# Optimization experiments

Hardware: AMD Instinct MI355X
Metric: run time of the kernel (lower is better)

Reference implementation:

```python
import jax, jax.numpy as jnp
import numpy as np

B = 32; L = 512; D_MODEL = 512; N_LAYERS = 4
D_STATE = 64; D_CONV = 4; EXPAND = 2; HEADDIM = 64; PRED = 96
D_INNER = EXPAND * D_MODEL            # 1024
NHEADS = D_INNER // HEADDIM           # 16
CONV_DIM = D_INNER + 2 * D_STATE      # 1152
D_IN_PROJ = 2 * D_INNER + 2 * D_STATE + NHEADS  # 2192
EPS = 1e-5


def setup_inputs() -> dict:
    key = jax.random.key(0)
    ks = jax.random.split(key, 8)
    s = lambda k, shape, scale=0.02: jax.random.normal(k, shape, jnp.float32) * scale
    return {
        "x": jax.random.normal(ks[0], (B, L, D_MODEL), jnp.float32),
        "in_proj_w": s(ks[1], (N_LAYERS, D_IN_PROJ, D_MODEL)),
        "conv_w": s(ks[2], (N_LAYERS, CONV_DIM, D_CONV), 0.2),
        "conv_b": jnp.zeros((N_LAYERS, CONV_DIM), jnp.float32),
        "dt_bias": jnp.log(jnp.expm1(jax.random.uniform(ks[3], (N_LAYERS, NHEADS), minval=0.001, maxval=0.1))),
        "A_log": jnp.log(jax.random.uniform(ks[4], (N_LAYERS, NHEADS), minval=1.0, maxval=16.0)),
        "Dp": jnp.ones((N_LAYERS, NHEADS), jnp.float32),
        "norm_w": jnp.ones((N_LAYERS, D_INNER), jnp.float32),
        "out_proj_w": s(ks[5], (N_LAYERS, D_MODEL, D_INNER)),
        "ln_w": jnp.ones((N_LAYERS, D_MODEL), jnp.float32),
        "ln_b": jnp.zeros((N_LAYERS, D_MODEL), jnp.float32),
        "final_w": s(ks[6], (D_MODEL, D_MODEL)),
        "final_b": jnp.zeros((D_MODEL,), jnp.float32),
    }


def _silu(x):
    return x * jax.nn.sigmoid(x)


def _causal_dwconv(x, w, b):
    # x: (B, L, C); depthwise causal conv, kernel D_CONV, left pad D_CONV-1
    xt = jnp.swapaxes(x, 1, 2)  # (B, C, L)
    y = jax.lax.conv_general_dilated(
        xt, w[:, None, :], window_strides=(1,), padding=[(D_CONV - 1, 0)],
        feature_group_count=CONV_DIM, dimension_numbers=("NCH", "OIH", "NCH"))
    return jnp.swapaxes(y + b[None, :, None], 1, 2)


def _ssd_scan(xh, dt, Bm, Cm, A, Dp):
    # xh: (B,L,H,P), dt: (B,L,H), Bm/Cm: (B,L,N), A/Dp: (H,)
    dA = jnp.exp(dt * A)  # (B,L,H)

    def step(h, t):
        dA_t, x_t, dt_t, B_t, C_t = t  # (B,H), (B,H,P), (B,H), (B,N), (B,N)
        h = h * dA_t[:, :, None, None] + (dt_t[:, :, None] * x_t)[..., None] * B_t[:, None, None, :]
        y = jnp.einsum("bhpn,bn->bhp", h, C_t)
        return h, y

    Bb, Ll, H, P = xh.shape
    N = Bm.shape[-1]
    h0 = jnp.zeros((Bb, H, P, N), xh.dtype)
    xs = (jnp.moveaxis(dA, 1, 0), jnp.moveaxis(xh, 1, 0), jnp.moveaxis(dt, 1, 0),
          jnp.moveaxis(Bm, 1, 0), jnp.moveaxis(Cm, 1, 0))
    _, ys = jax.lax.scan(step, h0, xs)
    y = jnp.moveaxis(ys, 0, 1)  # (B,L,H,P)
    return y + xh * Dp[None, None, :, None]


def _mamba2(x, w_in, cw, cb, dtb, a_log, dp, nw, w_out):
    zxbcdt = jnp.einsum("bld,ed->ble", x, w_in)  # (B,L,D_IN_PROJ)
    z = zxbcdt[..., :D_INNER]
    xBC = zxbcdt[..., D_INNER:D_INNER + CONV_DIM]
    dt = jax.nn.softplus(zxbcdt[..., -NHEADS:] + dtb)
    xBC = _silu(_causal_dwconv(xBC, cw, cb))
    xh = xBC[..., :D_INNER].reshape(x.shape[0], x.shape[1], NHEADS, HEADDIM)
    Bm = xBC[..., D_INNER:D_INNER + D_STATE]
    Cm = xBC[..., D_INNER + D_STATE:]
    A = -jnp.exp(a_log)
    y = _ssd_scan(xh, dt, Bm, Cm, A, dp).reshape(x.shape[0], x.shape[1], D_INNER)
    # gated RMSNorm (norm_before_gate=False): gate first, then normalize
    y = y * _silu(z)
    y = y * jax.lax.rsqrt(jnp.mean(y * y, axis=-1, keepdims=True) + EPS) * nw
    return jnp.einsum("ble,de->bld", y, w_out)


def _layernorm(x, w, b):
    xc = x - jnp.mean(x, axis=-1, keepdims=True)
    return xc * jax.lax.rsqrt(jnp.mean(xc * xc, axis=-1, keepdims=True) + EPS) * w + b


def reference(x, in_proj_w, conv_w, conv_b, dt_bias, A_log, Dp, norm_w,
              out_proj_w, ln_w, ln_b, final_w, final_b):
    h = x
    for i in range(N_LAYERS):
        res = h
        h = _mamba2(h, in_proj_w[i], conv_w[i], conv_b[i], dt_bias[i],
                    A_log[i], Dp[i], norm_w[i], out_proj_w[i])
        h = _layernorm(h + res, ln_w[i], ln_b[i])
        # dropout is identity in eval mode
    h = h[:, -PRED:, :]
    return jnp.einsum("bld,ed->ble", h, final_w) + final_b
```

## Files before the change

### kernel.cpp

```cpp
#include <hip/hip_runtime.h>
#include <stdint.h>

#define BATCH 32
#define SEQ   512
#define DM    512
#define NL    4
#define DSTATE 64
#define DI    1024
#define NH    16
#define HD    64
#define PREDN 96
#define CDIM  1152
#define CSEG  144
#define DPROJ 2192
#define XBW   1168
#define NC    8
#define EPSF  1e-5f

typedef float  f32x4  __attribute__((ext_vector_type(4)));
typedef __bf16 bf16x4 __attribute__((ext_vector_type(4)));
typedef __bf16 bf16x8 __attribute__((ext_vector_type(8)));

__device__ __forceinline__ float sigmoidf_(float x){ return 1.f/(1.f+__expf(-x)); }
__device__ __forceinline__ float siluf_(float x){ return x*sigmoidf_(x); }
__device__ __forceinline__ float softplusf_(float x){ return (x>20.f)?x:log1pf(__expf(x)); }

__device__ __forceinline__ void gld16(const void* g, void* l){
  __builtin_amdgcn_global_load_lds((__attribute__((address_space(1))) void*)g,
                                   (__attribute__((address_space(3))) void*)l, 16, 0, 0);
}

template<typename TC>
__global__ __launch_bounds__(256) void gemm128(
    const __bf16* __restrict__ A, const __bf16* __restrict__ W,
    TC* __restrict__ C, TC* __restrict__ C2, const float* __restrict__ bias,
    int M, int Nreal, int ldc, int ldc2, int splitN, int K, int remapA)
{
  __shared__ __bf16 sAB[2*128*64];
  __bf16* sA = sAB;
  __bf16* sW = sAB + 128*64;
  const int tid  = threadIdx.x;
  const int m0   = blockIdx.x*128, n0 = blockIdx.y*128;
  const int lane = tid&63, wave = tid>>6;
  const int l15  = lane&15, quad = lane>>4;
  const int wr   = (wave>>1)*64, wc = (wave&1)*64;
  f32x4 acc[4][4];
  #pragma unroll
  for (int a=0;a<4;++a)
    #pragma unroll
    for (int b=0;b<4;++b) acc[a][b] = (f32x4){0,0,0,0};

  for (int k0=0; k0<K; k0+=64){
    #pragma unroll
    for (int j=0;j<4;++j){
      const int f = j*256 + tid;
      const int r = f>>3;
      const int kc = (((f&7) ^ (r&7)))*8;
      int ga = m0 + r;
      if (remapA){ int bb = ga/PREDN; ga = bb*SEQ + (SEQ-PREDN) + (ga - bb*PREDN); }
      gld16(A + (size_t)ga*K + k0 + kc, &sA[f*8]);
      int rb = n0 + r; rb = rb < Nreal ? rb : (Nreal-1);
      gld16(W + (size_t)rb*K + k0 + kc, &sW[f*8]);
    }
    __syncthreads();
    #pragma unroll
    for (int kk=0; kk<64; kk+=32){
      const int kcb = (kk>>3) + quad;
      bf16x8 av[4], bv[4];
      #pragma unroll
      for (int mi=0;mi<4;++mi){
        const int row = wr+mi*16+l15;
        av[mi] = *(const bf16x8*)&sA[row*64 + ((kcb ^ (row&7))<<3)];
      }
      #pragma unroll
      for (int ni=0;ni<4;++ni){
        const int row = wc+ni*16+l15;
        bv[ni] = *(const bf16x8*)&sW[row*64 + ((kcb ^ (row&7))<<3)];
      }
      #pragma unroll
      for (int mi=0;mi<4;++mi)
        #pragma unroll
        for (int ni=0;ni<4;++ni)
          acc[mi][ni] = __builtin_amdgcn_mfma_f32_16x16x32_bf16(av[mi],bv[ni],acc[mi][ni],0,0,0);
    }
    __syncthreads();
  }

  if constexpr (sizeof(TC)==2){
    #pragma unroll
    for (int mi=0;mi<4;++mi)
      #pragma unroll
      for (int ni=0;ni<4;++ni)
        #pragma unroll
        for (int r4=0;r4<4;++r4){
          const int row = wr+mi*16+quad*4+r4;
          const int col = wc+ni*16+l15;
          const int g2  = (col>>3) ^ (row&15);
          sAB[row*128 + g2*8 + (col&7)] = (__bf16)acc[mi][ni][r4];
        }
    __syncthreads();
    #pragma unroll
    for (int it=0; it<8; ++it){
      const int idx = it*256 + tid;
      const int row = idx>>4, g = idx&15;
      const int g2 = g ^ (row&15);
      bf16x8 v = *(const bf16x8*)&sAB[row*128 + g2*8];
      const int col0 = n0 + g*8;
      if (col0 < Nreal){
        const int grow = m0 + row;
        if (col0 < splitN) *(bf16x8*)&C [(size_t)grow*ldc  + col0]          = v;
        else               *(bf16x8*)&C2[(size_t)grow*ldc2 + (col0-splitN)] = v;
      }
    }
  } else {
    #pragma unroll
    for (int ni=0;ni<4;++ni){
      const int col = n0 + wc + ni*16 + l15;
      if (col < Nreal){
        const float badd = bias ? bias[col] : 0.f;
        #pragma unroll
        for (int mi=0;mi<4;++mi){
          #pragma unroll
          for (int r4=0;r4<4;++r4){
            const int row = m0 + wr + mi*16 + quad*4 + r4;
            C[(size_t)row*ldc + col] = (TC)(acc[mi][ni][r4] + badd);
          }
        }
      }
    }
  }
}

__global__ __launch_bounds__(256) void cast4_k(
    const float* __restrict__ s0, __bf16* __restrict__ d0, int n0,
    const float* __restrict__ s1, __bf16* __restrict__ d1, int n1,
    const float* __restrict__ s2, __bf16* __restrict__ d2, int n2,
    const float* __restrict__ s3, __bf16* __restrict__ d3, int n3)
{
  int i = blockIdx.x*256 + threadIdx.x;
  const float* s; __bf16* d;
  if (i < n0){ s=s0; d=d0; }
  else if ((i-=n0) < n1){ s=s1; d=d1; }
  else if ((i-=n1) < n2){ s=s2; d=d2; }
  else if ((i-=n2) < n3){ s=s3; d=d3; }
  else return;
  float4 v = ((const float4*)s)[i];
  bf16x4 o;
  o[0]=(__bf16)v.x; o[1]=(__bf16)v.y; o[2]=(__bf16)v.z; o[3]=(__bf16)v.w;
  ((bf16x4*)d)[i] = o;
}

__global__ __launch_bounds__(256) void conv_silu_k(
    const __bf16* __restrict__ xbw, const float* __restrict__ cw,
    const float* __restrict__ cb, __bf16* __restrict__ xout,
    __bf16* __restrict__ bcout)
{
  int idx = blockIdx.x*256 + threadIdx.x;
  if (idx >= BATCH*SEQ*CSEG) return;
  const int seg = idx % CSEG;
  const int bt  = idx / CSEG;
  const int t = bt % SEQ, b = bt / SEQ;
  const int d0 = seg*8;
  const __bf16* src = xbw + ((size_t)b*SEQ + t)*XBW + d0;
  bf16x8 z8;
  #pragma unroll
  for (int e=0;e<8;++e) z8[e]=(__bf16)0.f;
  bf16x8 x3 = *(const bf16x8*)src;
  bf16x8 x2 = (t>=1)? *(const bf16x8*)(src -   XBW) : z8;
  bf16x8 x1 = (t>=2)? *(const bf16x8*)(src - 2*XBW) : z8;
  bf16x8 x0 = (t>=3)? *(const bf16x8*)(src - 3*XBW) : z8;
  const float4* w4  = (const float4*)(cw + (size_t)d0*4);
  const float4* cb4 = (const float4*)(cb + d0);
  float4 cbl = cb4[0], cbh = cb4[1];
  bf16x8 o;
  #pragma unroll
  for (int e=0;e<8;++e){
    float4 w = w4[e];
    float acc = (e<4 ? (&cbl.x)[e] : (&cbh.x)[e-4])
              + w.x*(float)x0[e] + w.y*(float)x1[e]
              + w.z*(float)x2[e] + w.w*(float)x3[e];
    o[e] = (__bf16)siluf_(acc);
  }
  if (d0 < DI) *(bf16x8*)(xout  + ((size_t)b*SEQ+t)*DI  + d0)       = o;
  else         *(bf16x8*)(bcout + ((size_t)b*SEQ+t)*128 + (d0-DI))  = o;
}

__global__ __launch_bounds__(256) void ssd_fused_k(
    const __bf16* __restrict__ bc,
    __bf16* __restrict__ xy,
    const __bf16* __restrict__ xbw,
    const float* __restrict__ dtb_, const float* __restrict__ alog_,
    const float* __restrict__ dp_)
{
  __shared__ __bf16 sPool[5*64*72];
  __bf16* sB   = sPool;
  __bf16* sS   = sPool;
  __bf16* sC   = sPool + 1*64*72;
  __bf16* sXT  = sPool + 2*64*72;
  __bf16* sBwT = sPool + 3*64*72;
  __bf16* sHT  = sPool + 4*64*72;
  __shared__ float sCS[SEQ], sDT[SEQ];
  const int bid = blockIdx.x;
  const int h = bid & 15, b = bid >> 4;
  const int tid = threadIdx.x, wave = tid>>6, lane = tid&63;
  const int l15 = lane&15, quad = lane>>4;
  const int wm = (wave>>1)*32, wn = (wave&1)*32;

  const float Ah  = -__expf(alog_[h]);
  const float dtb = dtb_[h];
  const float Dh  = dp_[h];

  for (int t = tid; t < SEQ; t += 256){
    float raw = (float)xbw[((size_t)b*SEQ + t)*XBW + CDIM + h];
    float dt = softplusf_(raw + dtb);
    sDT[t] = dt;
    sCS[t] = dt*Ah;
  }
  __syncthreads();
  for (int ch = wave; ch < NC; ch += 4){
    float s = sCS[ch*64 + lane];
    #pragma unroll
    for (int off=1; off<64; off<<=1){
      float v = __shfl_up(s, off);
      if (lane >= off) s += v;
    }
    sCS[ch*64 + lane] = s;
  }
  __syncthreads();

  f32x4 run[2][2];
  #pragma unroll
  for (int a=0;a<2;++a)
    #pragma unroll
    for (int d=0;d<2;++d) run[a][d] = (f32x4){0,0,0,0};

  for (int c = 0; c < NC; ++c){
    const int t0 = c*64;
    {
      const int r = tid>>2, seg = (tid&3)*16;
      const __bf16* row = bc + ((size_t)b*SEQ + t0 + r)*128;
      bf16x8 vb0 = *(const bf16x8*)(row + seg);
      bf16x8 vb1 = *(const bf16x8*)(row + seg + 8);
      bf16x8 vc0 = *(const bf16x8*)(row + 64 + seg);
      bf16x8 vc1 = *(const bf16x8*)(row + 64 + seg + 8);
      *(bf16x8*)&sB[r*72+seg]   = vb0;
      *(bf16x8*)&sB[r*72+seg+8] = vb1;
      *(bf16x8*)&sC[r*72+seg]   = vc0;
      *(bf16x8*)&sC[r*72+seg+8] = vc1;
      const float w = __expf(sCS[t0+63] - sCS[t0+r]) * sDT[t0+r];
      #pragma unroll
      for (int e=0;e<8;++e){
        sBwT[(seg+e)*72 + r]   = (__bf16)(w*(float)vb0[e]);
        sBwT[(seg+8+e)*72 + r] = (__bf16)(w*(float)vb1[e]);
      }
      const __bf16* xrow = xy + ((size_t)b*SEQ + t0 + r)*DI + h*64;
      bf16x8 vx0 = *(const bf16x8*)(xrow + seg);
      bf16x8 vx1 = *(const bf16x8*)(xrow + seg + 8);
      #pragma unroll
      for (int e=0;e<8;++e){
        sXT[(seg+e)*72 + r]   = vx0[e];
        sXT[(seg+8+e)*72 + r] = vx1[e];
      }
    }
    __syncthreads();

    f32x4 aS[2][2];
    #pragma unroll
    for (int a=0;a<2;++a)
      #pragma unroll
      for (int d=0;d<2;++d) aS[a][d] = (f32x4){0,0,0,0};
    #pragma unroll
    for (int kk=0; kk<64; kk+=32){
      const int kf = kk + quad*8;
      bf16x8 a0 = *(const bf16x8*)&sC[(wm+l15)*72+kf];
      bf16x8 a1 = *(const bf16x8*)&sC[(wm+16+l15)*72+kf];
      bf16x8 b0 = *(const bf16x8*)&sB[(wn+l15)*72+kf];
      bf16x8 b1 = *(const bf16x8*)&sB[(wn+16+l15)*72+kf];
      aS[0][0] = __builtin_amdgcn_mfma_f32_16x16x32_bf16(a0,b0,aS[0][0],0,0,0);
      aS[0][1] = __builtin_amdgcn_mfma_f32_16x16x32_bf16(a0,b1,aS[0][1],0,0,0);
      aS[1][0] = __builtin_amdgcn_mfma_f32_16x16x32_bf16(a1,b0,aS[1][0],0,0,0);
      aS[1][1] = __builtin_amdgcn_mfma_f32_16x16x32_bf16(a1,b1,aS[1][1],0,0,0);
    }
    __syncthreads();

    #pragma unroll
    for (int mi=0;mi<2;++mi)
      #pragma unroll
      for (int ni=0;ni<2;++ni)
        #pragma unroll
        for (int r4=0;r4<4;++r4){
          const int i = wm+mi*16+quad*4+r4, j = wn+ni*16+l15;
          float ed = __expf(fminf(sCS[t0+i]-sCS[t0+j], 0.f)) * sDT[t0+j];
          float v = aS[mi][ni][r4]*ed;
          sS[i*72+j] = (__bf16)((j<=i)? v : 0.f);
          sHT[j*72+i] = (__bf16)run[mi][ni][r4];
        }
    __syncthreads();

    f32x4 aY[2][2], aH[2][2], aYi[2][2];
    #pragma unroll
    for (int a=0;a<2;++a)
      #pragma unroll
      for (int d=0;d<2;++d){
        aY[a][d]=(f32x4){0,0,0,0}; aH[a][d]=(f32x4){0,0,0,0};
        aYi[a][d]=(f32x4){0,0,0,0};
      }
    #pragma unroll
    for (int kk=0; kk<64; kk+=32){
      const int kf = kk + quad*8;
      bf16x8 b0 = *(const bf16x8*)&sXT[(wn+l15)*72+kf];
      bf16x8 b1 = *(const bf16x8*)&sXT[(wn+16+l15)*72+kf];
      bf16x8 s0 = *(const bf16x8*)&sS[(wm+l15)*72+kf];
      bf16x8 s1 = *(const bf16x8*)&sS[(wm+16+l15)*72+kf];
      bf16x8 w0 = *(const bf16x8*)&sBwT[(wm+l15)*72+kf];
      bf16x8 w1 = *(const bf16x8*)&sBwT[(wm+16+l15)*72+kf];
      bf16x8 c0 = *(const bf16x8*)&sC[(wm+l15)*72+kf];
      bf16x8 c1 = *(const bf16x8*)&sC[(wm+16+l15)*72+kf];
      bf16x8 h0 = *(const bf16x8*)&sHT[(wn+l15)*72+kf];
      bf16x8 h1 = *(const bf16x8*)&sHT[(wn+16+l15)*72+kf];
      aY[0][0] = __builtin_amdgcn_mfma_f32_16x16x32_bf16(s0,b0,aY[0][0],0,0,0);
      aY[0][1] = __builtin_amdgcn_mfma_f32_16x16x32_bf16(s0,b1,aY[0][1],0,0,0);
      aY[1][0] = __builtin_amdgcn_mfma_f32_16x16x32_bf16(s1,b0,aY[1][0],0,0,0);
      aY[1][1] = __builtin_amdgcn_mfma_f32_16x16x32_bf16(s1,b1,aY[1][1],0,0,0);
      aH[0][0] = __builtin_amdgcn_mfma_f32_16x16x32_bf16(w0,b0,aH[0][0],0,0,0);
      aH[0][1] = __builtin_amdgcn_mfma_f32_16x16x32_bf16(w0,b1,aH[0][1],0,0,0);
      aH[1][0] = __builtin_amdgcn_mfma_f32_16x16x32_bf16(w1,b0,aH[1][0],0,0,0);
      aH[1][1] = __builtin_amdgcn_mfma_f32_16x16x32_bf16(w1,b1,aH[1][1],0,0,0);
      aYi[0][0] = __builtin_amdgcn_mfma_f32_16x16x32_bf16(c0,h0,aYi[0][0],0,0,0);
      aYi[0][1] = __builtin_amdgcn_mfma_f32_16x16x32_bf16(c0,h1,aYi[0][1],0,0,0);
      aYi[1][0] = __builtin_amdgcn_mfma_f32_16x16x32_bf16(c1,h0,aYi[1][0],0,0,0);
      aYi[1][1] = __builtin_amdgcn_mfma_f32_16x16x32_bf16(c1,h1,aYi[1][1],0,0,0);
    }

    const float lam = __expf(sCS[t0+63]);
    #pragma unroll
    for (int mi=0;mi<2;++mi)
      #pragma unroll
      for (int ni=0;ni<2;++ni)
        #pragma unroll
        for (int r4=0;r4<4;++r4){
          const int i = wm+mi*16+quad*4+r4;
          const int p = wn+ni*16+l15;
          const float xval = (float)sXT[p*72 + i];
          const float e2 = __expf(sCS[t0+i]);
          const float yv = aY[mi][ni][r4] + Dh*xval + e2*aYi[mi][ni][r4];
          xy[((size_t)b*SEQ + t0 + i)*DI + h*64 + p] = (__bf16)yv;
          run[mi][ni][r4] = run[mi][ni][r4]*lam + aH[mi][ni][r4];
        }
    __syncthreads();
  }
}

__global__ __launch_bounds__(256) void gate_rms_k(
    __bf16* __restrict__ y, const __bf16* __restrict__ z, const float* __restrict__ nw)
{
  __shared__ float red[4];
  const int tid = threadIdx.x;
  const int sub = tid>>7;
  const int off = (tid&127)*8;
  const size_t row = (size_t)blockIdx.x*2 + sub;
  __bf16* yrow = y + row*DI;
  const __bf16* zrow = z + row*DI;
  bf16x8 yv = *(const bf16x8*)(yrow+off);
  bf16x8 zv = *(const bf16x8*)(zrow+off);
  float u[8]; float ss = 0.f;
  #pragma unroll
  for (int e=0;e<8;++e){
    float uu = (float)yv[e]*siluf_((float)zv[e]);
    u[e]=uu; ss += uu*uu;
  }
  #pragma unroll
  for (int o=32;o;o>>=1) ss += __shfl_xor(ss,o);
  if ((tid&63)==0) red[tid>>6] = ss;
  __syncthreads();
  ss = red[sub*2] + red[sub*2+1];
  const float sc = rsqrtf(ss*(1.f/DI) + EPSF);
  const float4* nw4 = (const float4*)(nw + off);
  float4 n0 = nw4[0], n1 = nw4[1];
  bf16x8 o;
  #pragma unroll
  for (int e=0;e<8;++e)
    o[e] = (__bf16)(u[e]*sc*(e<4 ? (&n0.x)[e] : (&n1.x)[e-4]));
  *(bf16x8*)(yrow+off) = o;
}

__global__ __launch_bounds__(256) void add_ln_k(
    const __bf16* __restrict__ tmp, __bf16* __restrict__ resio,
    const float* __restrict__ w, const float* __restrict__ bb)
{
  const int tid = threadIdx.x, lane = tid&63;
  const size_t row = (size_t)blockIdx.x*4 + (tid>>6);
  const int off = lane*8;
  const __bf16* trow = tmp + row*DM;
  __bf16* rrow = resio + row*DM;
  bf16x8 tv = *(const bf16x8*)(trow+off);
  bf16x8 rv = *(const bf16x8*)(rrow+off);
  float v[8]; float s = 0.f;
  #pragma unroll
  for (int e=0;e<8;++e){ v[e]=(float)tv[e]+(float)rv[e]; s += v[e]; }
  #pragma unroll
  for (int o=32;o;o>>=1) s += __shfl_xor(s,o);
  const float mean = s*(1.f/DM);
  float q = 0.f;
  #pragma unroll
  for (int e=0;e<8;++e){ v[e]-=mean; q += v[e]*v[e]; }
  #pragma unroll
  for (int o=32;o;o>>=1) q += __shfl_xor(q,o);
  const float rstd = rsqrtf(q*(1.f/DM) + EPSF);
  const float4* w4 = (const float4*)(w + off);
  const float4* b4 = (const float4*)(bb + off);
  float4 w0=w4[0], w1=w4[1], b0=b4[0], b1=b4[1];
  bf16x8 o8;
  #pragma unroll
  for (int e=0;e<8;++e){
    float we = e<4 ? (&w0.x)[e] : (&w1.x)[e-4];
    float be = e<4 ? (&b0.x)[e] : (&b1.x)[e-4];
    o8[e] = (__bf16)(v[e]*rstd*we + be);
  }
  *(bf16x8*)(rrow+off) = o8;
}

extern "C" void kernel_launch(void* const* d_in, const int* in_sizes, int n_in,
                              void* d_out, int out_size, void* d_ws, size_t ws_size,
                              hipStream_t stream)
{
  const float* x         = (const float*)d_in[0];
  const float* in_proj_w = (const float*)d_in[1];
  const float* conv_w    = (const float*)d_in[2];
  const float* conv_b    = (const float*)d_in[3];
  const float* dt_bias   = (const float*)d_in[4];
  const float* A_log     = (const float*)d_in[5];
  const float* Dp        = (const float*)d_in[6];
  const float* norm_w    = (const float*)d_in[7];
  const float* out_proj_w= (const float*)d_in[8];
  const float* ln_w      = (const float*)d_in[9];
  const float* ln_b      = (const float*)d_in[10];
  const float* final_w   = (const float*)d_in[11];
  const float* final_b   = (const float*)d_in[12];
  float* out = (float*)d_out;

  const size_t ROWS = (size_t)BATCH*SEQ;
  __bf16* wbf_in  = (__bf16*)d_ws;
  __bf16* wbf_out = wbf_in  + (size_t)NL*DPROJ*DM;
  __bf16* wbf_fin = wbf_out + (size_t)NL*DM*DI;
  __bf16* zbuf    = wbf_fin + (size_t)DM*DM;
  __bf16* xbw     = zbuf    + ROWS*DI;
  __bf16* ybuf    = xbw     + ROWS*XBW;
  __bf16* bcb     = ybuf    + ROWS*DI;
  __bf16* xcur    = bcb     + ROWS*128;
  __bf16* tmp  = xbw;

  {
    int n1 = NL*DPROJ*DM/4, n2 = NL*DM*DI/4, n3 = DM*DM/4, n4 = (int)(ROWS*DM/4);
    int tot = n1+n2+n3+n4;
    cast4_k<<<(tot+255)/256, 256, 0, stream>>>(
        in_proj_w, wbf_in, n1, out_proj_w, wbf_out, n2,
        final_w, wbf_fin, n3, x, xcur, n4);
  }

  const int convTotal = BATCH*SEQ*CSEG;
  const int BIGN = 1<<30;

  for (int l=0; l<NL; ++l){
    const __bf16* wl = wbf_in + (size_t)l*DPROJ*DM;
    gemm128<__bf16><<<dim3((int)(ROWS/128), (DPROJ+127)/128), 256, 0, stream>>>(
        xcur, wl, zbuf, xbw, nullptr, (int)ROWS, DPROJ, DI, XBW, DI, DM, 0);
    conv_silu_k<<<(convTotal+255)/256, 256, 0, stream>>>(
        xbw, conv_w + (size_t)l*CDIM*4, conv_b + (size_t)l*CDIM, ybuf, bcb);
    ssd_fused_k<<<BATCH*NH, 256, 0, stream>>>(
        bcb, ybuf, xbw, dt_bias + l*NH, A_log + l*NH, Dp + l*NH);
    gate_rms_k<<<(int)(ROWS/2), 256, 0, stream>>>(ybuf, zbuf, norm_w + (size_t)l*DI);
    gemm128<__bf16><<<dim3((int)(ROWS/128), DM/128), 256, 0, stream>>>(
        ybuf, wbf_out + (size_t)l*DM*DI, tmp, tmp, nullptr, (int)ROWS, DM, DM, DM, BIGN, DI, 0);
    add_ln_k<<<(int)(ROWS/4), 256, 0, stream>>>(tmp, xcur, ln_w + l*DM, ln_b + l*DM);
  }
  gemm128<float><<<dim3((BATCH*PREDN)/128, DM/128), 256, 0, stream>>>(
      xcur, wbf_fin, out, out, final_b, BATCH*PREDN, DM, DM, DM, BIGN, DM, 1);
}
```

Before: 833.3 us.

## Add 256x256 tiled bf16 GEMM with phased prefetch for input projection

Introduces a 512-thread GEMM kernel with 256x256 output tiles, double-buffered LDS fed by direct global-to-LDS loads, XOR-swizzled shared layout, and a four-phase loop that interleaves prefetch of the next K tiles with MFMA work. The output is staged through swizzled LDS for vectorized stores split between the z and xBC buffers. It is used for the in_proj GEMM to raise arithmetic intensity per tile and cut global traffic. In exchange it uses far fewer blocks and wastes work on the padded last N tile, which may hurt occupancy and load balance.

Result: slower. 910.6 us (+9.3%).

```diff
diff --git a/kernel.cpp b/kernel.cpp
--- a/kernel.cpp
+++ b/kernel.cpp
@@ -28,6 +28,146 @@
 __device__ __forceinline__ void gld16(const void* g, void* l){
   __builtin_amdgcn_global_load_lds((__attribute__((address_space(1))) void*)g,
                                    (__attribute__((address_space(3))) void*)l, 16, 0, 0);
+}
+
+__global__ __launch_bounds__(512,2) void gemm256(
+    const __bf16* __restrict__ A, const __bf16* __restrict__ W,
+    __bf16* __restrict__ C, __bf16* __restrict__ C2,
+    int Nreal, int ldc, int ldc2, int splitN, int K)
+{
+  __shared__ __bf16 sm[2][2][256*64];
+  const int tid  = threadIdx.x;
+  const int m0   = blockIdx.x*256, n0 = blockIdx.y*256;
+  const int lane = tid&63, wave = tid>>6;
+  const int l15  = lane&15, quad = lane>>4;
+  const int wm   = wave>>2, wn = wave&3;
+  const int rA   = wm*128,  rB = wn*64;
+  const int nt   = K>>6;
+
+  f32x4 acc[8][4];
+  #pragma unroll
+  for (int a=0;a<8;++a)
+    #pragma unroll
+    for (int b=0;b<4;++b) acc[a][b] = (f32x4){0,0,0,0};
+
+  auto stA = [&](int bsel, int q0, int kt){
+    __bf16* dst = &sm[bsel][0][0];
+    const int k0 = kt*64;
+    #pragma unroll
+    for (int j=0;j<2;++j){
+      const int s  = j*512 + tid;
+      const int rl = s>>3, pb = s&7;
+      const int row = ((rl&64)<<1) + q0*64 + (rl&63);
+      const int kc  = (pb ^ (row&7))<<3;
+      gld16(A + (size_t)(m0+row)*K + k0 + kc, dst + row*64 + pb*8);
+    }
+  };
+  auto stB = [&](int bsel, int q1, int kt){
+    __bf16* dst = &sm[bsel][1][0];
+    const int k0 = kt*64;
+    #pragma unroll
+    for (int j=0;j<2;++j){
+      const int s  = j*512 + tid;
+      const int rl = s>>3, pb = s&7;
+      const int row = ((rl>>5)<<6) + q1*32 + (rl&31);
+      const int kc  = (pb ^ (row&7))<<3;
+      int gr = n0 + row; gr = gr < Nreal ? gr : Nreal-1;
+      gld16(W + (size_t)gr*K + k0 + kc, dst + row*64 + pb*8);
+    }
+  };
+
+  stA(0,0,0); stB(0,0,0); stA(0,1,0); stB(0,1,0);
+  if (nt > 1){
+    stA(1,0,1); stB(1,0,1);
+    asm volatile("s_waitcnt vmcnt(4)" ::: "memory");
+  } else {
+    asm volatile("s_waitcnt vmcnt(0)" ::: "memory");
+  }
+  asm volatile("" ::: "memory");
+  __builtin_amdgcn_s_barrier();
+  asm volatile("" ::: "memory");
+
+  for (int t=0; t<nt; ++t){
+    const int ct = t&1, nb = ct^1;
+    const __bf16* bA = &sm[ct][0][0];
+    const __bf16* bB = &sm[ct][1][0];
+    #pragma unroll
+    for (int ph=0; ph<4; ++ph){
+      const int q0 = ph>>1, q1 = ph&1;
+      bf16x8 av[4][2], bv[2][2];
+      #pragma unroll
+      for (int j=0;j<4;++j){
+        const int row = rA + q0*64 + j*16 + l15;
+        #pragma unroll
+        for (int kh=0;kh<2;++kh){
+          const int pbk = ((kh*4+quad) ^ (row&7))<<3;
+          av[j][kh] = *(const bf16x8*)&bA[row*64 + pbk];
+        }
+      }
+      #pragma unroll
+      for (int i=0;i<2;++i){
+        const int row = rB + q1*32 + i*16 + l15;
+        #pragma unroll
+        for (int kh=0;kh<2;++kh){
+          const int pbk = ((kh*4+quad) ^ (row&7))<<3;
+          bv[i][kh] = *(const bf16x8*)&bB[row*64 + pbk];
+        }
+      }
+      if      (ph==0){ if (t+1<nt) stA(nb,1,t+1); }
+      else if (ph==1){ if (t+1<nt) stB(nb,1,t+1); }
+      else if (ph==2){ if (t+2<nt) stA(ct,0,t+2); }
+      else           { if (t+2<nt) stB(ct,0,t+2); }
+      asm volatile("" ::: "memory");
+      __builtin_amdgcn_s_barrier();
+      asm volatile("" ::: "memory");
+      __builtin_amdgcn_s_setprio(1);
+      #pragma unroll
+      for (int kh=0;kh<2;++kh)
+        #pragma unroll
+        for (int j=0;j<4;++j)
+          #pragma unroll
+          for (int i=0;i<2;++i)
+            acc[q0*4+j][q1*2+i] = __builtin_amdgcn_mfma_f32_16x16x32_bf16(
+                av[j][kh], bv[i][kh], acc[q0*4+j][q1*2+i], 0,0,0);
+      __builtin_amdgcn_s_setprio(0);
+      if (ph==3){
+        if (t+2<nt) asm volatile("s_waitcnt vmcnt(4)" ::: "memory");
+        else        asm volatile("s_waitcnt vmcnt(0)" ::: "memory");
+      }
+      asm volatile("" ::: "memory");
+      __builtin_amdgcn_s_barrier();
+      asm volatile("" ::: "memory");
+    }
+  }
+
+  __bf16* sOut = &sm[0][0][0];
+  #pragma unroll
+  for (int mi=0;mi<8;++mi)
+    #pragma unroll
+    for (int ni=0;ni<4;++ni)
+      #pragma unroll
+      for (int r4=0;r4<4;++r4){
+        const int row = rA + mi*16 + quad*4 + r4;
+        const int col = rB + ni*16 + l15;
+        const int g2  = (col>>3) ^ (row&31);
+        sOut[row*256 + g2*8 + (col&7)] = (__bf16)acc[mi][ni][r4];
+      }
+  asm volatile("" ::: "memory");
+  __builtin_amdgcn_s_barrier();
+  asm volatile("" ::: "memory");
+  #pragma unroll
+  for (int it=0; it<16; ++it){
+    const int idx = it*512 + tid;
+    const int row = idx>>5, gp = idx&31;
+    const int gl  = gp ^ (row&31);
+    bf16x8 v = *(const bf16x8*)&sOut[row*256 + gp*8];
+    const int col0 = n0 + gl*8;
+    if (col0 < Nreal){
+      const int grow = m0 + row;
+      if (col0 < splitN) *(bf16x8*)&C [(size_t)grow*ldc  + col0]          = v;
+      else               *(bf16x8*)&C2[(size_t)grow*ldc2 + (col0-splitN)] = v;
+    }
+  }
 }
 
 template<typename TC>
@@ -463,8 +603,8 @@
 
   for (int l=0; l<NL; ++l){
     const __bf16* wl = wbf_in + (size_t)l*DPROJ*DM;
-    gemm128<__bf16><<<dim3((int)(ROWS/128), (DPROJ+127)/128), 256, 0, stream>>>(
-        xcur, wl, zbuf, xbw, nullptr, (int)ROWS, DPROJ, DI, XBW, DI, DM, 0);
+    gemm256<<<dim3((int)(ROWS/256), (DPROJ+255)/256), 512, 0, stream>>>(
+        xcur, wl, zbuf, xbw, DPROJ, DI, XBW, DI, DM);
     conv_silu_k<<<(convTotal+255)/256, 256, 0, stream>>>(
         xbw, conv_w + (size_t)l*CDIM*4, conv_b + (size_t)l*CDIM, ybuf, bcb);
     ssd_fused_k<<<BATCH*NH, 256, 0, stream>>>(
```

## Fuse out_proj GEMM with residual add and LayerNorm in one kernel

Applied to the files above, without the earlier changes.

Replaces the out_proj GEMM plus separate add+LayerNorm kernel with a single kernel. Each 512-thread block computes a full 64x512 row tile over K=1024 with double-buffered swizzled LDS staging, then adds the residual and reduces the row mean and variance across waves through shared memory. This removes the bf16 temporary round trip and one launch. In exchange it uses a large LDS footprint (about 147KB), which limits occupancy, and only 256 blocks are launched. Variance is now computed as E[x^2]-mean^2, which is less numerically robust than the two-pass form.

Result: slower. 859.0 us (+3.1%).

```diff
diff --git a/kernel.cpp b/kernel.cpp
--- a/kernel.cpp
+++ b/kernel.cpp
@@ -129,6 +129,126 @@
       }
     }
   }
+}
+
+__global__ __launch_bounds__(512) void gemm_ln_k(
+    const __bf16* __restrict__ A,
+    const __bf16* __restrict__ W,
+    __bf16* __restrict__ R,
+    const float* __restrict__ lw, const float* __restrict__ lb)
+{
+  __shared__ __bf16 sm[2][(64+512)*64];
+  __shared__ float sLN[4][64][2];
+  const int tid  = threadIdx.x;
+  const int m0   = blockIdx.x*64;
+  const int lane = tid&63;
+  const int wave = tid>>6;
+  const int l15  = lane&15, quad = lane>>4;
+  const int wm   = wave>>2, wn = wave&3;
+  const int nt   = DI/64;
+
+  f32x4 acc[2][8];
+  #pragma unroll
+  for (int a=0;a<2;++a)
+    #pragma unroll
+    for (int b=0;b<8;++b) acc[a][b] = (f32x4){0,0,0,0};
+
+  auto stage = [&](int bsel, int kt){
+    __bf16* dA = &sm[bsel][0];
+    __bf16* dB = &sm[bsel][64*64];
+    const int k0 = kt*64;
+    {
+      const int rl = tid>>3, pb = tid&7;
+      const int kc = (pb ^ (rl&7))<<3;
+      gld16(A + (size_t)(m0+rl)*DI + k0 + kc, dA + rl*64 + pb*8);
+    }
+    #pragma unroll
+    for (int j=0;j<8;++j){
+      const int s  = j*512 + tid;
+      const int rl = s>>3, pb = s&7;
+      const int kc = (pb ^ (rl&7))<<3;
+      gld16(W + (size_t)rl*DI + k0 + kc, dB + rl*64 + pb*8);
+    }
+  };
+
+  stage(0, 0);
+  asm volatile("s_waitcnt vmcnt(0)" ::: "memory");
+  __builtin_amdgcn_s_barrier();
+  asm volatile("" ::: "memory");
+
+  for (int t=0; t<nt; ++t){
+    const int ct = t&1;
+    if (t+1<nt) stage(ct^1, t+1);
+    asm volatile("" ::: "memory");
+    const __bf16* bA = &sm[ct][0];
+    const __bf16* bB = &sm[ct][64*64];
+    #pragma unroll
+    for (int kk=0; kk<2; ++kk){
+      const int kcb = kk*4 + quad;
+      bf16x8 av[2], bv[8];
+      #pragma unroll
+      for (int mi=0;mi<2;++mi){
+        const int row = wm*32 + mi*16 + l15;
+        av[mi] = *(const bf16x8*)&bA[row*64 + ((kcb ^ (row&7))<<3)];
+      }
+      #pragma unroll
+      for (int ni=0;ni<8;++ni){
+        const int row = wn*128 + ni*16 + l15;
+        bv[ni] = *(const bf16x8*)&bB[row*64 + ((kcb ^ (row&7))<<3)];
+      }
+      #pragma unroll
+      for (int mi=0;mi<2;++mi)
+        #pragma unroll
+        for (int ni=0;ni<8;++ni)
+          acc[mi][ni] = __builtin_amdgcn_mfma_f32_16x16x32_bf16(av[mi],bv[ni],acc[mi][ni],0,0,0);
+    }
+    if (t+1<nt) asm volatile("s_waitcnt vmcnt(0)" ::: "memory");
+    asm volatile("" ::: "memory");
+    __builtin_amdgcn_s_barrier();
+    asm volatile("" ::: "memory");
+  }
+
+  float lwv[8], lbv[8];
+  #pragma unroll
+  for (int ni=0;ni<8;++ni){
+    const int col = wn*128 + ni*16 + l15;
+    lwv[ni] = lw[col]; lbv[ni] = lb[col];
+  }
+  #pragma unroll
+  for (int mi=0;mi<2;++mi)
+    #pragma unroll
+    for (int r4=0;r4<4;++r4){
+      const int lr = wm*32 + mi*16 + quad*4 + r4;
+      const size_t rg = (size_t)(m0 + lr)*DM;
+      float s = 0.f, q = 0.f;
+      #pragma unroll
+      for (int ni=0;ni<8;++ni){
+        const int col = wn*128 + ni*16 + l15;
+        float v = acc[mi][ni][r4] + (float)R[rg + col];
+        acc[mi][ni][r4] = v;
+        s += v; q += v*v;
+      }
+      #pragma unroll
+      for (int o=1;o<16;o<<=1){ s += __shfl_xor(s,o); q += __shfl_xor(q,o); }
+      if (l15==0){ sLN[wn][lr][0] = s; sLN[wn][lr][1] = q; }
+    }
+  __syncthreads();
+  #pragma unroll
+  for (int mi=0;mi<2;++mi)
+    #pragma unroll
+    for (int r4=0;r4<4;++r4){
+      const int lr = wm*32 + mi*16 + quad*4 + r4;
+      const float S = sLN[0][lr][0]+sLN[1][lr][0]+sLN[2][lr][0]+sLN[3][lr][0];
+      const float Q = sLN[0][lr][1]+sLN[1][lr][1]+sLN[2][lr][1]+sLN[3][lr][1];
+      const float mean = S*(1.f/DM);
+      const float rstd = rsqrtf(fmaxf(Q*(1.f/DM) - mean*mean, 0.f) + EPSF);
+      const size_t rg = (size_t)(m0 + lr)*DM;
+      #pragma unroll
+      for (int ni=0;ni<8;++ni){
+        const int col = wn*128 + ni*16 + l15;
+        R[rg + col] = (__bf16)((acc[mi][ni][r4] - mean)*rstd*lwv[ni] + lbv[ni]);
+      }
+    }
 }
 
 __global__ __launch_bounds__(256) void cast4_k(
@@ -384,42 +504,6 @@
   *(bf16x8*)(yrow+off) = o;
 }
 
-__global__ __launch_bounds__(256) void add_ln_k(
-    const __bf16* __restrict__ tmp, __bf16* __restrict__ resio,
-    const float* __restrict__ w, const float* __restrict__ bb)
-{
-  const int tid = threadIdx.x, lane = tid&63;
-  const size_t row = (size_t)blockIdx.x*4 + (tid>>6);
-  const int off = lane*8;
-  const __bf16* trow = tmp + row*DM;
-  __bf16* rrow = resio + row*DM;
-  bf16x8 tv = *(const bf16x8*)(trow+off);
-  bf16x8 rv = *(const bf16x8*)(rrow+off);
-  float v[8]; float s = 0.f;
-  #pragma unroll
-  for (int e=0;e<8;++e){ v[e]=(float)tv[e]+(float)rv[e]; s += v[e]; }
-  #pragma unroll
-  for (int o=32;o;o>>=1) s += __shfl_xor(s,o);
-  const float mean = s*(1.f/DM);
-  float q = 0.f;
-  #pragma unroll
-  for (int e=0;e<8;++e){ v[e]-=mean; q += v[e]*v[e]; }
-  #pragma unroll
-  for (int o=32;o;o>>=1) q += __shfl_xor(q,o);
-  const float rstd = rsqrtf(q*(1.f/DM) + EPSF);
-  const float4* w4 = (const float4*)(w + off);
-  const float4* b4 = (const float4*)(bb + off);
-  float4 w0=w4[0], w1=w4[1], b0=b4[0], b1=b4[1];
-  bf16x8 o8;
-  #pragma unroll
-  for (int e=0;e<8;++e){
-    float we = e<4 ? (&w0.x)[e] : (&w1.x)[e-4];
-    float be = e<4 ? (&b0.x)[e] : (&b1.x)[e-4];
-    o8[e] = (__bf16)(v[e]*rstd*we + be);
-  }
-  *(bf16x8*)(rrow+off) = o8;
-}
-
 extern "C" void kernel_launch(void* const* d_in, const int* in_sizes, int n_in,
                               void* d_out, int out_size, void* d_ws, size_t ws_size,
                               hipStream_t stream)
@@ -448,7 +532,6 @@
   __bf16* ybuf    = xbw     + ROWS*XBW;
   __bf16* bcb     = ybuf    + ROWS*DI;
   __bf16* xcur    = bcb     + ROWS*128;
-  __bf16* tmp  = xbw;
 
   {
     int n1 = NL*DPROJ*DM/4, n2 = NL*DM*DI/4, n3 = DM*DM/4, n4 = (int)(ROWS*DM/4);
@@ -470,9 +553,8 @@
     ssd_fused_k<<<BATCH*NH, 256, 0, stream>>>(
         bcb, ybuf, xbw, dt_bias + l*NH, A_log + l*NH, Dp + l*NH);
     gate_rms_k<<<(int)(ROWS/2), 256, 0, stream>>>(ybuf, zbuf, norm_w + (size_t)l*DI);
-    gemm128<__bf16><<<dim3((int)(ROWS/128), DM/128), 256, 0, stream>>>(
-        ybuf, wbf_out + (size_t)l*DM*DI, tmp, tmp, nullptr, (int)ROWS, DM, DM, DM, BIGN, DI, 0);
-    add_ln_k<<<(int)(ROWS/4), 256, 0, stream>>>(tmp, xcur, ln_w + l*DM, ln_b + l*DM);
+    gemm_ln_k<<<(int)(ROWS/64), 512, 0, stream>>>(
+        ybuf, wbf_out + (size_t)l*DM*DI, xcur, ln_w + l*DM, ln_b + l*DM);
   }
   gemm128<float><<<dim3((BATCH*PREDN)/128, DM/128), 256, 0, stream>>>(
       xcur, wbf_fin, out, out, final_b, BATCH*PREDN, DM, DM, DM, BIGN, DM, 1);
```
